# Optimization experiments

Hardware: AMD Instinct MI355X
Metric: run time of the kernel (lower is better)

## Reference

```python
import math
import jax, jax.numpy as jnp
import numpy as np

B, C, H, W = 32, 256, 32, 32  # in==mid==out channels

def setup_inputs() -> dict:
    key = jax.random.key(0)
    ks = jax.random.split(key, 3)
    x = jax.random.normal(ks[0], (B, C, H, W), dtype=jnp.float32)
    # 1x1 convs are just channel matmuls: weight [out_ch, in_ch]
    w_in = jax.random.normal(ks[1], (3 * C, C), dtype=jnp.float32) * (1.0 / math.sqrt(C))
    b_in = jnp.zeros((3 * C,), dtype=jnp.float32)
    # project_out has init_scale=0.0 in the original; we use random weights so the
    # output (and gradients) are non-trivial, but the math is identical.
    w_out = jax.random.normal(ks[2], (C, C), dtype=jnp.float32) * (1.0 / math.sqrt(C))
    b_out = jnp.zeros((C,), dtype=jnp.float32)
    return {"x": x, "w_in": w_in, "b_in": b_in, "w_out": w_out, "b_out": b_out}

def _qkv_attention(q, k, v):
    # q,k,v: [B,C,H,W]. Full spatial self-attention over the HxW grid.
    b, c, h, w = q.shape
    scores = jnp.einsum('bchw,bcHW->bhwHW', q, k)          # [B,H,W,H,W]
    scores = scores.reshape(b, h, w, h * w) / math.sqrt(c)
    attn = jax.nn.softmax(scores, axis=-1).reshape(b, h, w, h, w)
    return jnp.einsum('bhwHW,bcHW->bchw', attn, v)          # [B,C,H,W]

def reference(x, w_in, b_in, w_out, b_out):
    skip = x  # in_channels == out_channels -> Identity skip
    qkv = jnp.einsum('oc,bchw->bohw', w_in, x) + b_in[None, :, None, None]
    q, k, v = jnp.split(qkv, 3, axis=1)
    h = _qkv_attention(q, k, v)
    out = jnp.einsum('oc,bchw->bohw', w_out, h) + b_out[None, :, None, None]
    return out + skip
```

## Files before the change

### kernel.cpp

```cpp
#include <hip/hip_runtime.h>
#include <hip/hip_bf16.h>

typedef __attribute__((ext_vector_type(8))) short bf16x8;
typedef __attribute__((ext_vector_type(4))) float f32x4;
typedef __attribute__((ext_vector_type(16))) float f32x16;
typedef long long i64;

#define NB 32
#define NC 256
#define NN 1024

__device__ __forceinline__ unsigned pack2(float a, float b) {
    __hip_bfloat16 ha = __float2bfloat16(a), hb = __float2bfloat16(b);
    unsigned short ua = *(unsigned short*)&ha, ub = *(unsigned short*)&hb;
    return (unsigned)ua | ((unsigned)ub << 16);
}

__device__ __forceinline__ float bflo(unsigned u) {
    union { unsigned i; float f; } x; x.i = u << 16; return x.f;
}
__device__ __forceinline__ float bfhi(unsigned u) {
    union { unsigned i; float f; } x; x.i = u & 0xffff0000u; return x.f;
}
__device__ __forceinline__ unsigned fp8x4(float a, float b, float c, float d) {
    int w = __builtin_amdgcn_cvt_pk_fp8_f32(a, b, 0, false);
    w = __builtin_amdgcn_cvt_pk_fp8_f32(c, d, w, true);
    return (unsigned)w;
}

__device__ __forceinline__ void glds16(const void* g, void* lds) {
    __builtin_amdgcn_global_load_lds(
        (const __attribute__((address_space(1))) unsigned int*)g,
        (__attribute__((address_space(3))) unsigned int*)lds, 16, 0, 0);
}

__global__ __launch_bounds__(256) void xpose_kernel(
    const float* __restrict__ x, __hip_bfloat16* __restrict__ Xt)
{
    __shared__ float Ls[64 * 67];
    const int t = threadIdx.x;
    const int n0 = blockIdx.x * 64, c0 = blockIdx.y * 64, b = blockIdx.z;
    const int cl = t >> 4, nl = (t & 15) * 4;
    const float* xb = x + ((size_t)b * NC + c0) * NN + n0;
    #pragma unroll
    for (int q4 = 0; q4 < 4; ++q4) {
        const int c = cl + q4 * 16;
        const float4 v = *(const float4*)(xb + (size_t)c * NN + nl);
        Ls[(nl + 0) * 67 + c] = v.x;
        Ls[(nl + 1) * 67 + c] = v.y;
        Ls[(nl + 2) * 67 + c] = v.z;
        Ls[(nl + 3) * 67 + c] = v.w;
    }
    __syncthreads();
    #pragma unroll
    for (int p = 0; p < 2; ++p) {
        const int idx = p * 256 + t, n = idx >> 3, cs = idx & 7;
        const float* r = &Ls[n * 67 + cs * 8];
        uint4 o;
        o.x = pack2(r[0], r[1]); o.y = pack2(r[2], r[3]);
        o.z = pack2(r[4], r[5]); o.w = pack2(r[6], r[7]);
        *(uint4*)(Xt + ((size_t)b * NN + n0 + n) * NC + c0 + cs * 8) = o;
    }
}

__device__ __forceinline__ void stage_ab(const __hip_bfloat16* __restrict__ Ag,
                                         const float* __restrict__ Bg,
                                         char* Ad, char* Bd, int ks, int t)
{
    const int srow = t >> 3, spch = t & 7;
    #pragma unroll
    for (int it = 0; it < 4; ++it) {
        const int row = it * 32 + srow;
        const int sw  = row & 7;
        glds16(Ag + (size_t)row * NC + ks * 64 + ((spch ^ sw) << 3),
               Ad + (it * 256 + t) * 16);
        const float* wp = Bg + (size_t)row * NC + ks * 64 + (spch << 3);
        const float4 u0 = *(const float4*)wp;
        const float4 u1 = *(const float4*)(wp + 4);
        uint4 pk;
        pk.x = pack2(u0.x, u0.y); pk.y = pack2(u0.z, u0.w);
        pk.z = pack2(u1.x, u1.y); pk.w = pack2(u1.z, u1.w);
        *(uint4*)(Bd + row * 128 + ((spch ^ sw) << 4)) = pk;
    }
}

__global__ __launch_bounds__(256, 2) void qkv_gemm_kernel(
    const __hip_bfloat16* __restrict__ Xt, const float* __restrict__ w_in,
    const float* __restrict__ b_in, unsigned char* __restrict__ Qt8,
    unsigned char* __restrict__ Kt8, unsigned char* __restrict__ Vf8)
{
    __shared__ char smem[65536];
    char* const A0 = smem;
    char* const A1 = smem + 16384;
    char* const B0 = smem + 32768;
    char* const B1 = smem + 49152;

    const int t  = threadIdx.x;
    const int wv = t >> 6, ln = t & 63, lo = ln & 15, hi = ln >> 4;
    const int wm = wv >> 1, wn = wv & 1;
    const int n0 = blockIdx.x * 128, o0 = blockIdx.y * 128, b = blockIdx.z;

    const __hip_bfloat16* Ag = Xt + ((size_t)b * NN + n0) * NC;
    const float* Bg = w_in + (size_t)o0 * NC;

    f32x4 acc[4][4];
    #pragma unroll
    for (int i = 0; i < 4; ++i)
        #pragma unroll
        for (int j = 0; j < 4; ++j) acc[i][j] = (f32x4){0.f, 0.f, 0.f, 0.f};

    int ra[4], rb[4];
    #pragma unroll
    for (int f = 0; f < 4; ++f) { ra[f] = wm * 64 + f * 16 + lo; rb[f] = wn * 64 + f * 16 + lo; }

    stage_ab(Ag, Bg, A0, B0, 0, t);
    __syncthreads();
    #pragma unroll
    for (int ks = 0; ks < 4; ++ks) {
        char* Ac = (ks & 1) ? A1 : A0;
        char* Bc = (ks & 1) ? B1 : B0;
        if (ks < 3)
            stage_ab(Ag, Bg, (ks & 1) ? A0 : A1, (ks & 1) ? B0 : B1, ks + 1, t);
        #pragma unroll
        for (int kk = 0; kk < 2; ++kk) {
            bf16x8 av[4], bv[4];
            #pragma unroll
            for (int f = 0; f < 4; ++f) {
                av[f] = *(const bf16x8*)(Ac + ra[f] * 128 + (((kk << 2) | hi) ^ (ra[f] & 7)) * 16);
                bv[f] = *(const bf16x8*)(Bc + rb[f] * 128 + (((kk << 2) | hi) ^ (rb[f] & 7)) * 16);
            }
            #pragma unroll
            for (int fm = 0; fm < 4; ++fm)
                #pragma unroll
                for (int fn = 0; fn < 4; ++fn)
                    acc[fm][fn] = __builtin_amdgcn_mfma_f32_16x16x32_bf16(
                        av[fm], bv[fn], acc[fm][fn], 0, 0, 0);
        }
        __syncthreads();
    }

    float bias[4];
    #pragma unroll
    for (int fn = 0; fn < 4; ++fn) bias[fn] = b_in[o0 + wn * 64 + fn * 16 + lo];

    __hip_bfloat16* Ls = (__hip_bfloat16*)smem;
    if (o0 < 512) {
        #pragma unroll
        for (int fm = 0; fm < 4; ++fm)
            #pragma unroll
            for (int fn = 0; fn < 4; ++fn)
                #pragma unroll
                for (int r = 0; r < 4; ++r)
                    Ls[(wm * 64 + fm * 16 + hi * 4 + r) * 136 + wn * 64 + fn * 16 + lo] =
                        __float2bfloat16(acc[fm][fn][r] + bias[fn]);
        __syncthreads();
        unsigned char* dst = (o0 < 256) ? Qt8 : Kt8;
        const int oc = (o0 < 256) ? o0 : o0 - 256;
        #pragma unroll
        for (int p = 0; p < 4; ++p) {
            const int idx = p * 256 + t, row = idx >> 3, ch = idx & 7;
            const unsigned* ls = (const unsigned*)&Ls[row * 136 + ch * 16];
            const uint4 a = *(const uint4*)ls;
            const uint4 b2 = *(const uint4*)(ls + 4);
            uint4 o;
            o.x = fp8x4(bflo(a.x), bfhi(a.x), bflo(a.y), bfhi(a.y));
            o.y = fp8x4(bflo(a.z), bfhi(a.z), bflo(a.w), bfhi(a.w));
            o.z = fp8x4(bflo(b2.x), bfhi(b2.x), bflo(b2.y), bfhi(b2.y));
            o.w = fp8x4(bflo(b2.z), bfhi(b2.z), bflo(b2.w), bfhi(b2.w));
            *(uint4*)(dst + ((size_t)b * NN + n0 + row) * 256 + oc + ch * 16) = o;
        }
    } else {
        #pragma unroll
        for (int fm = 0; fm < 4; ++fm)
            #pragma unroll
            for (int fn = 0; fn < 4; ++fn)
                #pragma unroll
                for (int r = 0; r < 4; ++r)
                    Ls[(wn * 64 + fn * 16 + lo) * 136 + wm * 64 + fm * 16 + hi * 4 + r] =
                        __float2bfloat16(acc[fm][fn][r] + bias[fn]);
        __syncthreads();
        #pragma unroll
        for (int p = 0; p < 8; ++p) {
            const int idx = p * 256 + t;
            const int ch = idx >> 7, cr = idx & 127;
            const unsigned* ls = (const unsigned*)&Ls[cr * 136 + ch * 8];
            const uint4 a = *(const uint4*)ls;
            uint2 o;
            o.x = fp8x4(bflo(a.x), bfhi(a.x), bflo(a.y), bfhi(a.y));
            o.y = fp8x4(bflo(a.z), bfhi(a.z), bflo(a.w), bfhi(a.w));
            const int g = (n0 >> 3) + ch;
            *(uint2*)(Vf8 + (((size_t)b * 128 + g) * 256 + (o0 - 512) + cr) * 8) = o;
        }
    }
}

__device__ __forceinline__ void stage_tile(const unsigned char* __restrict__ Kb,
                                           const unsigned char* __restrict__ Vb,
                                           char* Kd, char* Vd, int m0, int t)
{
    {
        const int row = t >> 4, pc = t & 15;
        const int prow = (row & 19) | ((row & 4) << 1) | ((row & 8) >> 1);
        const int sc = pc ^ (row & 15);
        glds16(Kb + (size_t)(m0 + prow) * 256 + sc * 16, Kd + t * 16);
    }
    {
        glds16(Vb + (size_t)(m0 >> 3) * 2048 + t * 16, Vd + t * 16);
    }
}

__global__ __launch_bounds__(512, 2) void attn_kernel(
    const unsigned char* __restrict__ Qt8, const unsigned char* __restrict__ Kt8,
    const unsigned char* __restrict__ Vf8, const float* __restrict__ w_out,
    const float* __restrict__ b_out, const float* __restrict__ xg,
    float* __restrict__ out)
{
    __shared__ char smem[139264];

    const int t  = threadIdx.x;
    const int wv = t >> 6, ln = t & 63;
    const int l32 = ln & 31, h2 = ln >> 5;
    const int qgrp = wv & 3, half = wv >> 2;
    const int wid = blockIdx.x + 8 * blockIdx.y;
    const int swz = (wid & 7) * 32 + (wid >> 3);
    const int qb = swz & 7, b = swz >> 3;
    const int n0 = qb * 128;
    const float scale = 0.0625f;

    const unsigned char* Kbase = Kt8 + (size_t)b * NN * 256;
    const unsigned char* Vbase = Vf8 + (size_t)b * 128 * 2048;

    const unsigned char* qp = Qt8 + ((size_t)b * NN + n0 + qgrp * 32 + l32) * 256;
    i64 qf[16];
    #pragma unroll
    for (int ks = 0; ks < 16; ++ks)
        qf[ks] = *(const i64*)(qp + ks * 16 + h2 * 8);

    f32x16 acc[8];
    #pragma unroll
    for (int ct = 0; ct < 8; ++ct)
        #pragma unroll
        for (int r = 0; r < 16; ++r) acc[ct][r] = 0.f;
    float mr = 0.f;
    float sr = 0.f;

    #pragma unroll
    for (int tt = 0; tt < 4; ++tt)
        stage_tile(Kbase, Vbase, smem + tt * 8192, smem + 32768 + tt * 8192,
                   tt * 32, t);
    __syncthreads();

    for (int s = 0; s < 16; ++s) {
        if (s < 15) {
            const int t2 = 2 * s + 2, t3 = 2 * s + 3;
            stage_tile(Kbase, Vbase, smem + (t2 & 3) * 8192,
                       smem + 32768 + (t2 & 3) * 8192, t2 * 32, t);
            stage_tile(Kbase, Vbase, smem + (t3 & 3) * 8192,
                       smem + 32768 + (t3 & 3) * 8192, t3 * 32, t);
        }
        const int tile = 2 * s + half;
        char* const Kc = smem + (tile & 3) * 8192;
        char* const Vc = smem + 32768 + (tile & 3) * 8192;

        f32x16 sfA, sfB;
        #pragma unroll
        for (int r = 0; r < 16; ++r) { sfA[r] = 0.f; sfB[r] = 0.f; }
        __builtin_amdgcn_s_setprio(1);
        #pragma unroll
        for (int ks = 0; ks < 8; ++ks) {
            const int pc = ks ^ (l32 & 15);
            const i64 kf = *(const i64*)(Kc + l32 * 256 + pc * 16 + h2 * 8);
            sfA = __builtin_amdgcn_mfma_f32_32x32x16_fp8_fp8(kf, qf[ks], sfA, 0, 0, 0);
        }
        #pragma unroll
        for (int ks = 8; ks < 16; ++ks) {
            const int pc = ks ^ (l32 & 15);
            const i64 kf = *(const i64*)(Kc + l32 * 256 + pc * 16 + h2 * 8);
            sfB = __builtin_amdgcn_mfma_f32_32x32x16_fp8_fp8(kf, qf[ks], sfB, 0, 0, 0);
        }
        __builtin_amdgcn_s_setprio(0);

        float sv[16];
        #pragma unroll
        for (int r = 0; r < 16; ++r) sv[r] = sfA[r] + sfB[r];

        float m0a = fmaxf(sv[0], sv[1]),  m1a = fmaxf(sv[2], sv[3]);
        float m2a = fmaxf(sv[4], sv[5]),  m3a = fmaxf(sv[6], sv[7]);
        float m4a = fmaxf(sv[8], sv[9]),  m5a = fmaxf(sv[10], sv[11]);
        float m6a = fmaxf(sv[12], sv[13]), m7a = fmaxf(sv[14], sv[15]);
        float m0b = fmaxf(m0a, m1a), m1b = fmaxf(m2a, m3a);
        float m2b = fmaxf(m4a, m5a), m3b = fmaxf(m6a, m7a);
        float tm = fmaxf(fmaxf(m0b, m1b), fmaxf(m2b, m3b));
        tm = fmaxf(tm, __shfl_xor(tm, 32, 64));
        tm *= scale;
        if (__any(tm > mr + 8.f)) {
            const float mn = fmaxf(mr, tm);
            const float al = __expf(mr - mn);
            mr = mn;
            sr *= al;
            #pragma unroll
            for (int ct = 0; ct < 8; ++ct)
                #pragma unroll
                for (int r = 0; r < 16; ++r) acc[ct][r] *= al;
        }
        float p[16];
        #pragma unroll
        for (int r = 0; r < 16; ++r)
            p[r] = __expf(sv[r] * scale - mr);
        float s0a = p[0] + p[1],  s1a = p[2] + p[3];
        float s2a = p[4] + p[5],  s3a = p[6] + p[7];
        float s4a = p[8] + p[9],  s5a = p[10] + p[11];
        float s6a = p[12] + p[13], s7a = p[14] + p[15];
        float sacc = ((s0a + s1a) + (s2a + s3a)) + ((s4a + s5a) + (s6a + s7a));
        sacc += __shfl_xor(sacc, 32, 64);
        sr += sacc;

        i64 pb[2];
        #pragma unroll
        for (int kstep = 0; kstep < 2; ++kstep) {
            union { unsigned u[2]; i64 l; } uu;
            uu.u[0] = fp8x4(p[8 * kstep + 0], p[8 * kstep + 1],
                            p[8 * kstep + 2], p[8 * kstep + 3]);
            uu.u[1] = fp8x4(p[8 * kstep + 4], p[8 * kstep + 5],
                            p[8 * kstep + 6], p[8 * kstep + 7]);
            pb[kstep] = uu.l;
        }

        __builtin_amdgcn_s_setprio(1);
        #pragma unroll
        for (int ct = 0; ct < 8; ++ct) {
            #pragma unroll
            for (int kstep = 0; kstep < 2; ++kstep) {
                const i64 vf = *(const i64*)(Vc + (2 * kstep + h2) * 2048 +
                                             (ct * 32 + l32) * 8);
                acc[ct] = __builtin_amdgcn_mfma_f32_32x32x16_fp8_fp8(vf, pb[kstep], acc[ct], 0, 0, 0);
            }
        }
        __builtin_amdgcn_s_setprio(0);
        __syncthreads();
    }

    float* const ex = (float*)smem;
    __hip_bfloat16* const Hld = (__hip_bfloat16*)(smem + 69632);
    #pragma unroll
    for (int ph = 0; ph < 2; ++ph) {
        if (half == 1 && (qgrp >> 1) == ph) {
            float* dst = ex + ((qgrp & 1) * 64 + ln) * 132;
            #pragma unroll
            for (int ct = 0; ct < 8; ++ct)
                #pragma unroll
                for (int rr = 0; rr < 4; ++rr) {
                    f32x4 v = {acc[ct][rr * 4 + 0], acc[ct][rr * 4 + 1],
                               acc[ct][rr * 4 + 2], acc[ct][rr * 4 + 3]};
                    *(f32x4*)(dst + ct * 16 + rr * 4) = v;
                }
            dst[128] = mr;
            dst[129] = sr;
        }
        __syncthreads();
        if (half == 0 && (qgrp >> 1) == ph) {
            const float* src = ex + ((qgrp & 1) * 64 + ln) * 132;
            const float mb = src[128], lb = src[129];
            const float m = fmaxf(mr, mb);
            float fa = __expf(mr - m), fb = __expf(mb - m);
            const float inv = 1.0f / (sr * fa + lb * fb);
            fa *= inv; fb *= inv;
            __hip_bfloat16* hrow = Hld + (size_t)(qgrp * 32 + l32) * 264;
            #pragma unroll
            for (int ct = 0; ct < 8; ++ct)
                #pragma unroll
                for (int ss = 0; ss < 4; ++ss) {
                    const float o0 = acc[ct][ss * 4 + 0] * fa + src[ct * 16 + ss * 4 + 0] * fb;
                    const float o1 = acc[ct][ss * 4 + 1] * fa + src[ct * 16 + ss * 4 + 1] * fb;
                    const float o2 = acc[ct][ss * 4 + 2] * fa + src[ct * 16 + ss * 4 + 2] * fb;
                    const float o3 = acc[ct][ss * 4 + 3] * fa + src[ct * 16 + ss * 4 + 3] * fb;
                    uint2 v;
                    v.x = pack2(o0, o1);
                    v.y = pack2(o2, o3);
                    *(uint2*)(hrow + ct * 32 + ss * 8 + h2 * 4) = v;
                }
        }
        __syncthreads();
    }

    __hip_bfloat16* const Wld = (__hip_bfloat16*)smem;
    const int oT = wv >> 1;
    const int nT0 = (wv & 1) * 2, nT1 = nT0 + 1;
    for (int oh = 0; oh < 2; ++oh) {
        #pragma unroll
        for (int p = 0; p < 8; ++p) {
            const int idx = p * 512 + t;
            const int o = idx >> 5, ck = idx & 31;
            const float* wp = w_out + (size_t)(oh * 128 + o) * NC + ck * 8;
            const float4 u0 = *(const float4*)wp;
            const float4 u1 = *(const float4*)(wp + 4);
            uint4 pk;
            pk.x = pack2(u0.x, u0.y); pk.y = pack2(u0.z, u0.w);
            pk.z = pack2(u1.x, u1.y); pk.w = pack2(u1.z, u1.w);
            *(uint4*)((char*)Wld + (size_t)o * 528 + ck * 16) = pk;
        }
        __syncthreads();

        f32x16 oc0, oc1;
        #pragma unroll
        for (int r = 0; r < 16; ++r) { oc0[r] = 0.f; oc1[r] = 0.f; }
        __builtin_amdgcn_s_setprio(1);
        #pragma unroll
        for (int ks = 0; ks < 16; ++ks) {
            const int ck = ks * 2 + h2;
            bf16x8 wf = *(const bf16x8*)((char*)Wld + (size_t)(oT * 32 + l32) * 528 + ck * 16);
            bf16x8 hf0 = *(const bf16x8*)((char*)Hld + (size_t)(nT0 * 32 + l32) * 528 + ck * 16);
            bf16x8 hf1 = *(const bf16x8*)((char*)Hld + (size_t)(nT1 * 32 + l32) * 528 + ck * 16);
            oc0 = __builtin_amdgcn_mfma_f32_32x32x16_bf16(wf, hf0, oc0, 0, 0, 0);
            oc1 = __builtin_amdgcn_mfma_f32_32x32x16_bf16(wf, hf1, oc1, 0, 0, 0);
        }
        __builtin_amdgcn_s_setprio(0);

        #pragma unroll
        for (int r = 0; r < 16; ++r) {
            const int o = oh * 128 + oT * 32 + (r & 3) + 8 * (r >> 2) + 4 * h2;
            const float bo = b_out[o];
            const size_t rowg = ((size_t)b * NC + o) * NN + n0;
            const size_t g0 = rowg + nT0 * 32 + l32;
            const size_t g1 = rowg + nT1 * 32 + l32;
            out[g0] = oc0[r] + bo + xg[g0];
            out[g1] = oc1[r] + bo + xg[g1];
        }
        __syncthreads();
    }
}

extern "C" void kernel_launch(void* const* d_in, const int* in_sizes, int n_in,
                              void* d_out, int out_size, void* d_ws, size_t ws_size,
                              hipStream_t stream) {
    const float* x     = (const float*)d_in[0];
    const float* w_in  = (const float*)d_in[1];
    const float* b_in  = (const float*)d_in[2];
    const float* w_out = (const float*)d_in[3];
    const float* b_out = (const float*)d_in[4];
    float* out = (float*)d_out;

    if (ws_size < (size_t)64 * 1024 * 1024) return;
    char* ws = (char*)d_ws;
    unsigned char* Qt8 = (unsigned char*)(ws);
    unsigned char* Kt8 = (unsigned char*)(ws + ((size_t)8 << 20));
    unsigned char* Vf8 = (unsigned char*)(ws + ((size_t)16 << 20));
    __hip_bfloat16* Xt = (__hip_bfloat16*)(ws + ((size_t)24 << 20));

    xpose_kernel<<<dim3(16, 4, 32), 256, 0, stream>>>(x, Xt);
    qkv_gemm_kernel<<<dim3(8, 6, 32), 256, 0, stream>>>(Xt, w_in, b_in, Qt8, Kt8, Vf8);
    attn_kernel<<<dim3(8, 32), 512, 0, stream>>>(Qt8, Kt8, Vf8, w_out, b_out, x, out);
}
```

Measured before the change: 88.03 us.

## Switch QKV projection GEMM to FP8 inputs and prefetch w_out in attention epilogue

The transposed activations are now written as FP8 instead of bf16, and the QKV projection GEMM converts w_in to FP8 and uses fp8 MFMA. This halves the intermediate and LDS traffic, so LDS shrinks and occupancy is raised to 3 blocks per CU. Separately, the attention kernel loads w_out into registers before the combine phase and double-stages the second half. This hides global load latency behind earlier work. The lower projection precision adds numerical error, and the extra registers could cause spills.

```diff
diff --git a/kernel.cpp b/kernel.cpp
--- a/kernel.cpp
+++ b/kernel.cpp
@@ -35,7 +35,7 @@
 }
 
 __global__ __launch_bounds__(256) void xpose_kernel(
-    const float* __restrict__ x, __hip_bfloat16* __restrict__ Xt)
+    const float* __restrict__ x, unsigned char* __restrict__ Xt8)
 {
     __shared__ float Ls[64 * 67];
     const int t = threadIdx.x;
@@ -56,51 +56,54 @@
     for (int p = 0; p < 2; ++p) {
         const int idx = p * 256 + t, n = idx >> 3, cs = idx & 7;
         const float* r = &Ls[n * 67 + cs * 8];
-        uint4 o;
-        o.x = pack2(r[0], r[1]); o.y = pack2(r[2], r[3]);
-        o.z = pack2(r[4], r[5]); o.w = pack2(r[6], r[7]);
-        *(uint4*)(Xt + ((size_t)b * NN + n0 + n) * NC + c0 + cs * 8) = o;
-    }
-}
-
-__device__ __forceinline__ void stage_ab(const __hip_bfloat16* __restrict__ Ag,
-                                         const float* __restrict__ Bg,
-                                         char* Ad, char* Bd, int ks, int t)
+        uint2 o;
+        o.x = fp8x4(r[0], r[1], r[2], r[3]);
+        o.y = fp8x4(r[4], r[5], r[6], r[7]);
+        *(uint2*)(Xt8 + ((size_t)b * NN + n0 + n) * 256 + c0 + cs * 8) = o;
+    }
+}
+
+__device__ __forceinline__ void stage_ab8(const unsigned char* __restrict__ Ag,
+                                          const float* __restrict__ Bg,
+                                          char* Ad, char* Bd, int ks, int t)
 {
-    const int srow = t >> 3, spch = t & 7;
-    #pragma unroll
-    for (int it = 0; it < 4; ++it) {
-        const int row = it * 32 + srow;
-        const int sw  = row & 7;
-        glds16(Ag + (size_t)row * NC + ks * 64 + ((spch ^ sw) << 3),
-               Ad + (it * 256 + t) * 16);
-        const float* wp = Bg + (size_t)row * NC + ks * 64 + (spch << 3);
+    #pragma unroll
+    for (int p = 0; p < 2; ++p) {
+        const int idx = p * 256 + t;
+        const int row = idx >> 2, pc = idx & 3;
+        const int lp = pc ^ (row & 3);
+        glds16(Ag + (size_t)row * 256 + ks * 64 + lp * 16, Ad + idx * 16);
+        const float* wp = Bg + (size_t)row * NC + ks * 64 + lp * 16;
         const float4 u0 = *(const float4*)wp;
         const float4 u1 = *(const float4*)(wp + 4);
+        const float4 u2 = *(const float4*)(wp + 8);
+        const float4 u3 = *(const float4*)(wp + 12);
         uint4 pk;
-        pk.x = pack2(u0.x, u0.y); pk.y = pack2(u0.z, u0.w);
-        pk.z = pack2(u1.x, u1.y); pk.w = pack2(u1.z, u1.w);
-        *(uint4*)(Bd + row * 128 + ((spch ^ sw) << 4)) = pk;
-    }
-}
-
-__global__ __launch_bounds__(256, 2) void qkv_gemm_kernel(
-    const __hip_bfloat16* __restrict__ Xt, const float* __restrict__ w_in,
+        pk.x = fp8x4(u0.x, u0.y, u0.z, u0.w);
+        pk.y = fp8x4(u1.x, u1.y, u1.z, u1.w);
+        pk.z = fp8x4(u2.x, u2.y, u2.z, u2.w);
+        pk.w = fp8x4(u3.x, u3.y, u3.z, u3.w);
+        *(uint4*)(Bd + idx * 16) = pk;
+    }
+}
+
+__global__ __launch_bounds__(256, 3) void qkv_gemm_kernel(
+    const unsigned char* __restrict__ Xt8, const float* __restrict__ w_in,
     const float* __restrict__ b_in, unsigned char* __restrict__ Qt8,
     unsigned char* __restrict__ Kt8, unsigned char* __restrict__ Vf8)
 {
-    __shared__ char smem[65536];
+    __shared__ char smem[34816];
     char* const A0 = smem;
-    char* const A1 = smem + 16384;
-    char* const B0 = smem + 32768;
-    char* const B1 = smem + 49152;
+    char* const A1 = smem + 8192;
+    char* const B0 = smem + 16384;
+    char* const B1 = smem + 24576;
 
     const int t  = threadIdx.x;
     const int wv = t >> 6, ln = t & 63, lo = ln & 15, hi = ln >> 4;
     const int wm = wv >> 1, wn = wv & 1;
     const int n0 = blockIdx.x * 128, o0 = blockIdx.y * 128, b = blockIdx.z;
 
-    const __hip_bfloat16* Ag = Xt + ((size_t)b * NN + n0) * NC;
+    const unsigned char* Ag = Xt8 + ((size_t)b * NN + n0) * 256;
     const float* Bg = w_in + (size_t)o0 * NC;
 
     f32x4 acc[4][4];
@@ -113,27 +116,27 @@
     #pragma unroll
     for (int f = 0; f < 4; ++f) { ra[f] = wm * 64 + f * 16 + lo; rb[f] = wn * 64 + f * 16 + lo; }
 
-    stage_ab(Ag, Bg, A0, B0, 0, t);
+    stage_ab8(Ag, Bg, A0, B0, 0, t);
     __syncthreads();
     #pragma unroll
     for (int ks = 0; ks < 4; ++ks) {
         char* Ac = (ks & 1) ? A1 : A0;
         char* Bc = (ks & 1) ? B1 : B0;
         if (ks < 3)
-            stage_ab(Ag, Bg, (ks & 1) ? A0 : A1, (ks & 1) ? B0 : B1, ks + 1, t);
+            stage_ab8(Ag, Bg, (ks & 1) ? A0 : A1, (ks & 1) ? B0 : B1, ks + 1, t);
         #pragma unroll
         for (int kk = 0; kk < 2; ++kk) {
-            bf16x8 av[4], bv[4];
+            i64 av[4], bv[4];
             #pragma unroll
             for (int f = 0; f < 4; ++f) {
-                av[f] = *(const bf16x8*)(Ac + ra[f] * 128 + (((kk << 2) | hi) ^ (ra[f] & 7)) * 16);
-                bv[f] = *(const bf16x8*)(Bc + rb[f] * 128 + (((kk << 2) | hi) ^ (rb[f] & 7)) * 16);
+                av[f] = *(const i64*)(Ac + ra[f] * 64 + (((kk << 2) | hi) ^ ((ra[f] & 3) << 1)) * 8);
+                bv[f] = *(const i64*)(Bc + rb[f] * 64 + (((kk << 2) | hi) ^ ((rb[f] & 3) << 1)) * 8);
             }
             #pragma unroll
             for (int fm = 0; fm < 4; ++fm)
                 #pragma unroll
                 for (int fn = 0; fn < 4; ++fn)
-                    acc[fm][fn] = __builtin_amdgcn_mfma_f32_16x16x32_bf16(
+                    acc[fm][fn] = __builtin_amdgcn_mfma_f32_16x16x32_fp8_fp8(
                         av[fm], bv[fn], acc[fm][fn], 0, 0, 0);
         }
         __syncthreads();
@@ -340,6 +343,16 @@
         __syncthreads();
     }
 
+    const int wo = t >> 5, wck = t & 31;
+    float4 wr[16];
+    #pragma unroll
+    for (int p = 0; p < 8; ++p) {
+        const int o = p * 16 + wo;
+        const float* wp = w_out + (size_t)o * NC + wck * 8;
+        wr[2 * p]     = *(const float4*)wp;
+        wr[2 * p + 1] = *(const float4*)(wp + 4);
+    }
+
     float* const ex = (float*)smem;
     __hip_bfloat16* const Hld = (__hip_bfloat16*)(smem + 69632);
     #pragma unroll
@@ -386,21 +399,26 @@
     __hip_bfloat16* const Wld = (__hip_bfloat16*)smem;
     const int oT = wv >> 1;
     const int nT0 = (wv & 1) * 2, nT1 = nT0 + 1;
+
+    #pragma unroll
+    for (int p = 0; p < 8; ++p) {
+        const int o = p * 16 + wo;
+        uint4 pk;
+        pk.x = pack2(wr[2*p].x, wr[2*p].y);     pk.y = pack2(wr[2*p].z, wr[2*p].w);
+        pk.z = pack2(wr[2*p+1].x, wr[2*p+1].y); pk.w = pack2(wr[2*p+1].z, wr[2*p+1].w);
+        *(uint4*)((char*)Wld + (size_t)o * 528 + wck * 16) = pk;
+    }
+    #pragma unroll
+    for (int p = 0; p < 8; ++p) {
+        const int o = 128 + p * 16 + wo;
+        const float* wp = w_out + (size_t)o * NC + wck * 8;
+        wr[2 * p]     = *(const float4*)wp;
+        wr[2 * p + 1] = *(const float4*)(wp + 4);
+    }
+    __syncthreads();
+
+    #pragma unroll
     for (int oh = 0; oh < 2; ++oh) {
-        #pragma unroll
-        for (int p = 0; p < 8; ++p) {
-            const int idx = p * 512 + t;
-            const int o = idx >> 5, ck = idx & 31;
-            const float* wp = w_out + (size_t)(oh * 128 + o) * NC + ck * 8;
-            const float4 u0 = *(const float4*)wp;
-            const float4 u1 = *(const float4*)(wp + 4);
-            uint4 pk;
-            pk.x = pack2(u0.x, u0.y); pk.y = pack2(u0.z, u0.w);
-            pk.z = pack2(u1.x, u1.y); pk.w = pack2(u1.z, u1.w);
-            *(uint4*)((char*)Wld + (size_t)o * 528 + ck * 16) = pk;
-        }
-        __syncthreads();
-
         f32x16 oc0, oc1;
         #pragma unroll
         for (int r = 0; r < 16; ++r) { oc0[r] = 0.f; oc1[r] = 0.f; }
@@ -427,6 +445,17 @@
             out[g1] = oc1[r] + bo + xg[g1];
         }
         __syncthreads();
+        if (oh == 0) {
+            #pragma unroll
+            for (int p = 0; p < 8; ++p) {
+                const int o = p * 16 + wo;
+                uint4 pk;
+                pk.x = pack2(wr[2*p].x, wr[2*p].y);     pk.y = pack2(wr[2*p].z, wr[2*p].w);
+                pk.z = pack2(wr[2*p+1].x, wr[2*p+1].y); pk.w = pack2(wr[2*p+1].z, wr[2*p+1].w);
+                *(uint4*)((char*)Wld + (size_t)o * 528 + wck * 16) = pk;
+            }
+            __syncthreads();
+        }
     }
 }
 
@@ -445,9 +474,9 @@
     unsigned char* Qt8 = (unsigned char*)(ws);
     unsigned char* Kt8 = (unsigned char*)(ws + ((size_t)8 << 20));
     unsigned char* Vf8 = (unsigned char*)(ws + ((size_t)16 << 20));
-    __hip_bfloat16* Xt = (__hip_bfloat16*)(ws + ((size_t)24 << 20));
-
-    xpose_kernel<<<dim3(16, 4, 32), 256, 0, stream>>>(x, Xt);
-    qkv_gemm_kernel<<<dim3(8, 6, 32), 256, 0, stream>>>(Xt, w_in, b_in, Qt8, Kt8, Vf8);
+    unsigned char* Xt8 = (unsigned char*)(ws + ((size_t)24 << 20));
+
+    xpose_kernel<<<dim3(16, 4, 32), 256, 0, stream>>>(x, Xt8);
+    qkv_gemm_kernel<<<dim3(8, 6, 32), 256, 0, stream>>>(Xt8, w_in, b_in, Qt8, Kt8, Vf8);
     attn_kernel<<<dim3(8, 32), 512, 0, stream>>>(Qt8, Kt8, Vf8, w_out, b_out, x, out);
 }
```

After: 84.37 us. 4.2% less time.
